# Kernel optimization log

Measured on AMD Instinct MI355X. Metric: run time of the kernel, lower is better.

Reference implementation:

```python
import jax, jax.numpy as jnp
import numpy as np


def setup_inputs() -> dict:
    key = jax.random.key(0)
    k1, k2, k3 = jax.random.split(key, 3)
    x = jax.random.normal(k1, (128, 3, 16, 64, 64), dtype=jnp.float32)
    conv_weight = jax.random.normal(k2, (24, 3, 3, 3, 3), dtype=jnp.float32) * 0.1
    conv_bias = jax.random.normal(k3, (24,), dtype=jnp.float32) * 0.1
    return {"x": x, "conv_weight": conv_weight, "conv_bias": conv_bias}


def reference(x, conv_weight, conv_bias):
    # Conv3d, stride=1, padding=0 (VALID), dilation=1, groups=1, NCDHW layout
    y = jax.lax.conv_general_dilated(
        x, conv_weight,
        window_strides=(1, 1, 1),
        padding='VALID',
        dimension_numbers=('NCDHW', 'OIDHW', 'NCDHW'),
    )
    y = y + conv_bias[None, :, None, None, None]  # [B, 24, 14, 62, 62]
    y = jnp.min(y, axis=2)                        # min over depth -> [B, 24, 62, 62]
    return jax.nn.softmax(y, axis=1)              # softmax over channels
```

## Files before the change

kernel.cpp:

```cpp
#include <hip/hip_runtime.h>
#include <math.h>

#define BATCH 128
#define CIN   3
#define DIN   16
#define HWIN  64
#define COUT  24
#define DOUT  14
#define HOUT  62
#define WOUT  62


__global__ __launch_bounds__(192, 3) void conv_min_softmax_v2(
    const float* __restrict__ x,
    const float* __restrict__ w,
    const float* __restrict__ bias,
    float* __restrict__ out)
{
    __shared__ __align__(16) float sx[3][9][68];
    __shared__ float sm[COUT][64];

    const int tid = threadIdx.x;
    const int bid = blockIdx.x;
    const int ho  = bid % HOUT;
    const int b   = bid / HOUT;

    const int co = tid >> 3;
    const int wg = tid & 7;

    const float* xb = x + (size_t)b * (CIN * DIN * HWIN * HWIN);

    float wreg[81];
    #pragma unroll
    for (int q = 0; q < 81; ++q) wreg[q] = w[co * 81 + q];
    const float bco = bias[co];

    const int r  = tid >> 6;
    const int wc = tid & 63;

    #pragma unroll
    for (int d = 0; d < 2; ++d) {
        #pragma unroll
        for (int cin = 0; cin < CIN; ++cin) {
            sx[d][cin * 3 + r][wc] =
                xb[(cin * DIN + d) * (HWIN * HWIN) + (ho + r) * HWIN + wc];
        }
    }

    float m[8];
    #pragma unroll
    for (int i = 0; i < 8; ++i) m[i] = 1e30f;

    #pragma unroll 1
    for (int dz = 0; dz < DOUT; ++dz) {
        const int s2 = (dz + 2) % 3;
        #pragma unroll
        for (int cin = 0; cin < CIN; ++cin) {
            sx[s2][cin * 3 + r][wc] =
                xb[(cin * DIN + dz + 2) * (HWIN * HWIN) + (ho + r) * HWIN + wc];
        }
        __syncthreads();

        const int p0 = dz % 3;
        const int p1 = (dz + 1) % 3;
        const float* planes[3] = { &sx[p0][0][0], &sx[p1][0][0], &sx[s2][0][0] };

        float acc[8];
        #pragma unroll
        for (int i = 0; i < 8; ++i) acc[i] = 0.f;

        #pragma unroll
        for (int kd = 0; kd < 3; ++kd) {
            const float* plane = planes[kd];
            #pragma unroll
            for (int cin = 0; cin < CIN; ++cin) {
                #pragma unroll
                for (int kh = 0; kh < 3; ++kh) {
                    const float* rp = plane + (cin * 3 + kh) * 68 + wg * 8;
                    float xr[10];
                    const float4 q0 = *(const float4*)(rp);
                    const float4 q1 = *(const float4*)(rp + 4);
                    const float2 q2 = *(const float2*)(rp + 8);
                    xr[0] = q0.x; xr[1] = q0.y; xr[2] = q0.z; xr[3] = q0.w;
                    xr[4] = q1.x; xr[5] = q1.y; xr[6] = q1.z; xr[7] = q1.w;
                    xr[8] = q2.x; xr[9] = q2.y;
                    #pragma unroll
                    for (int kw = 0; kw < 3; ++kw) {
                        const float wv = wreg[cin * 27 + kd * 9 + kh * 3 + kw];
                        #pragma unroll
                        for (int i = 0; i < 8; ++i)
                            acc[i] = fmaf(wv, xr[i + kw], acc[i]);
                    }
                }
            }
        }
        #pragma unroll
        for (int i = 0; i < 8; ++i) m[i] = fminf(m[i], acc[i]);
        __syncthreads();
    }

    #pragma unroll
    for (int i = 0; i < 8; ++i) sm[co][wg * 8 + i] = m[i] + bco;
    __syncthreads();

    if (tid < WOUT) {
        const int p = tid;
        float mx = -1e30f;
        #pragma unroll
        for (int c = 0; c < COUT; ++c) mx = fmaxf(mx, sm[c][p]);
        float e[COUT];
        float ssum = 0.f;
        #pragma unroll
        for (int c = 0; c < COUT; ++c) { e[c] = __expf(sm[c][p] - mx); ssum += e[c]; }
        const float inv = 1.f / ssum;
        float* ob = out + (size_t)b * COUT * (HOUT * WOUT) + ho * WOUT + p;
        #pragma unroll
        for (int c = 0; c < COUT; ++c) ob[(size_t)c * (HOUT * WOUT)] = e[c] * inv;
    }
}

extern "C" void kernel_launch(void* const* d_in, const int* in_sizes, int n_in,
                              void* d_out, int out_size, void* d_ws, size_t ws_size,
                              hipStream_t stream) {
    const float* x    = (const float*)d_in[0];
    const float* w    = (const float*)d_in[1];
    const float* bias = (const float*)d_in[2];
    float* out = (float*)d_out;

    const int blocks = BATCH * HOUT;
    conv_min_softmax_v2<<<blocks, 192, 0, stream>>>(x, w, bias, out);
}
```

Measured before the change: 457.0 us.

## Stream input depth planes once with rolling accumulators and register prefetch

The kernel now loads each input depth plane into shared memory once and applies all three depth taps of the weights to it. Three rolling accumulator sets (A0/A1/A2) are shifted after each plane instead of re-reading three planes per output depth. Global loads for the next plane are prefetched into registers while the current plane is computed, which overlaps load latency with math. Shared-memory reads drop by about 3x, but live registers grow (three 8-wide accumulators plus 81 weights) and the volatile weight loads may hurt occupancy or scheduling.

```diff
diff --git a/kernel.cpp b/kernel.cpp
--- a/kernel.cpp
+++ b/kernel.cpp
@@ -9,16 +9,56 @@
 #define DOUT  14
 #define HOUT  62
 #define WOUT  62
+#define HW2   (HWIN * HWIN)
 
 
-__global__ __launch_bounds__(192, 3) void conv_min_softmax_v2(
+template<bool KD0, bool KD1, bool KD2>
+__device__ __forceinline__ void conv_step(const float* sxp, int wg,
+                                          const float wreg[81],
+                                          float A0[8], float A1[8], float A2[8])
+{
+    #pragma unroll
+    for (int cin = 0; cin < 3; ++cin) {
+        #pragma unroll
+        for (int kh = 0; kh < 3; ++kh) {
+            const float* rp = sxp + (cin * 3 + kh) * 68 + wg * 8;
+            float xr[10];
+            const float4 q0 = *(const float4*)(rp);
+            const float4 q1 = *(const float4*)(rp + 4);
+            const float2 q2 = *(const float2*)(rp + 8);
+            xr[0] = q0.x; xr[1] = q0.y; xr[2] = q0.z; xr[3] = q0.w;
+            xr[4] = q1.x; xr[5] = q1.y; xr[6] = q1.z; xr[7] = q1.w;
+            xr[8] = q2.x; xr[9] = q2.y;
+            #pragma unroll
+            for (int kw = 0; kw < 3; ++kw) {
+                if (KD2) {
+                    const float wv = wreg[cin * 27 + 2 * 9 + kh * 3 + kw];
+                    #pragma unroll
+                    for (int i = 0; i < 8; ++i) A0[i] = fmaf(wv, xr[i + kw], A0[i]);
+                }
+                if (KD1) {
+                    const float wv = wreg[cin * 27 + 1 * 9 + kh * 3 + kw];
+                    #pragma unroll
+                    for (int i = 0; i < 8; ++i) A1[i] = fmaf(wv, xr[i + kw], A1[i]);
+                }
+                if (KD0) {
+                    const float wv = wreg[cin * 27 + 0 * 9 + kh * 3 + kw];
+                    #pragma unroll
+                    for (int i = 0; i < 8; ++i) A2[i] = fmaf(wv, xr[i + kw], A2[i]);
+                }
+            }
+        }
+    }
+}
+
+__global__ __launch_bounds__(192, 3) void conv_min_softmax_v3(
     const float* __restrict__ x,
     const float* __restrict__ w,
     const float* __restrict__ bias,
     float* __restrict__ out)
 {
-    __shared__ __align__(16) float sx[3][9][68];
-    __shared__ float sm[COUT][64];
+    __shared__ __align__(16) float sx[9 * 68];
+    __shared__ __align__(16) float sm[COUT][68];
 
     const int tid = threadIdx.x;
     const int bid = blockIdx.x;
@@ -28,76 +68,78 @@
     const int co = tid >> 3;
     const int wg = tid & 7;
 
-    const float* xb = x + (size_t)b * (CIN * DIN * HWIN * HWIN);
+    const float* xb = x + (size_t)b * (CIN * DIN * HW2);
 
     float wreg[81];
-    #pragma unroll
-    for (int q = 0; q < 81; ++q) wreg[q] = w[co * 81 + q];
+    {
+        volatile const float* wv = w + co * 81;
+        #pragma unroll
+        for (int q = 0; q < 81; ++q) wreg[q] = wv[q];
+    }
     const float bco = bias[co];
 
     const int r  = tid >> 6;
     const int wc = tid & 63;
 
+    float A0[8], A1[8], A2[8], m[8];
     #pragma unroll
-    for (int d = 0; d < 2; ++d) {
+    for (int i = 0; i < 8; ++i) { A0[i] = 0.f; A1[i] = 0.f; A2[i] = 0.f; m[i] = 1e30f; }
+
+    float g0, g1, g2, n0, n1, n2;
+    g0 = xb[(0 * DIN + 0) * HW2 + (ho + r) * HWIN + wc];
+    g1 = xb[(1 * DIN + 0) * HW2 + (ho + r) * HWIN + wc];
+    g2 = xb[(2 * DIN + 0) * HW2 + (ho + r) * HWIN + wc];
+
+#define STAGE_AND_PREFETCH(D)                                              \
+    sx[(0 * 3 + r) * 68 + wc] = g0;                                        \
+    sx[(1 * 3 + r) * 68 + wc] = g1;                                        \
+    sx[(2 * 3 + r) * 68 + wc] = g2;                                        \
+    if ((D) < DIN - 1) {                                                   \
+        n0 = xb[(0 * DIN + (D) + 1) * HW2 + (ho + r) * HWIN + wc];         \
+        n1 = xb[(1 * DIN + (D) + 1) * HW2 + (ho + r) * HWIN + wc];         \
+        n2 = xb[(2 * DIN + (D) + 1) * HW2 + (ho + r) * HWIN + wc];         \
+    }                                                                      \
+    __syncthreads();
+
+#define SHIFT()                                                            \
+    _Pragma("unroll")                                                      \
+    for (int i = 0; i < 8; ++i) { A0[i] = A1[i]; A1[i] = A2[i]; A2[i] = 0.f; } \
+    g0 = n0; g1 = n1; g2 = n2;
+
+    STAGE_AND_PREFETCH(0)
+    conv_step<true, false, false>(sx, wg, wreg, A0, A1, A2);
+    SHIFT()
+    __syncthreads();
+
+    STAGE_AND_PREFETCH(1)
+    conv_step<true, true, false>(sx, wg, wreg, A0, A1, A2);
+    SHIFT()
+    __syncthreads();
+
+    #pragma unroll 1
+    for (int d = 2; d <= 13; ++d) {
+        STAGE_AND_PREFETCH(d)
+        conv_step<true, true, true>(sx, wg, wreg, A0, A1, A2);
         #pragma unroll
-        for (int cin = 0; cin < CIN; ++cin) {
-            sx[d][cin * 3 + r][wc] =
-                xb[(cin * DIN + d) * (HWIN * HWIN) + (ho + r) * HWIN + wc];
-        }
+        for (int i = 0; i < 8; ++i) m[i] = fminf(m[i], A0[i]);
+        SHIFT()
+        __syncthreads();
     }
 
-    float m[8];
+    STAGE_AND_PREFETCH(14)
+    conv_step<false, true, true>(sx, wg, wreg, A0, A1, A2);
     #pragma unroll
-    for (int i = 0; i < 8; ++i) m[i] = 1e30f;
+    for (int i = 0; i < 8; ++i) m[i] = fminf(m[i], A0[i]);
+    SHIFT()
+    __syncthreads();
 
-    #pragma unroll 1
-    for (int dz = 0; dz < DOUT; ++dz) {
-        const int s2 = (dz + 2) % 3;
-        #pragma unroll
-        for (int cin = 0; cin < CIN; ++cin) {
-            sx[s2][cin * 3 + r][wc] =
-                xb[(cin * DIN + dz + 2) * (HWIN * HWIN) + (ho + r) * HWIN + wc];
-        }
-        __syncthreads();
+    STAGE_AND_PREFETCH(15)
+    conv_step<false, false, true>(sx, wg, wreg, A0, A1, A2);
+    #pragma unroll
+    for (int i = 0; i < 8; ++i) m[i] = fminf(m[i], A0[i]);
 
-        const int p0 = dz % 3;
-        const int p1 = (dz + 1) % 3;
-        const float* planes[3] = { &sx[p0][0][0], &sx[p1][0][0], &sx[s2][0][0] };
-
-        float acc[8];
-        #pragma unroll
-        for (int i = 0; i < 8; ++i) acc[i] = 0.f;
-
-        #pragma unroll
-        for (int kd = 0; kd < 3; ++kd) {
-            const float* plane = planes[kd];
-            #pragma unroll
-            for (int cin = 0; cin < CIN; ++cin) {
-                #pragma unroll
-                for (int kh = 0; kh < 3; ++kh) {
-                    const float* rp = plane + (cin * 3 + kh) * 68 + wg * 8;
-                    float xr[10];
-                    const float4 q0 = *(const float4*)(rp);
-                    const float4 q1 = *(const float4*)(rp + 4);
-                    const float2 q2 = *(const float2*)(rp + 8);
-                    xr[0] = q0.x; xr[1] = q0.y; xr[2] = q0.z; xr[3] = q0.w;
-                    xr[4] = q1.x; xr[5] = q1.y; xr[6] = q1.z; xr[7] = q1.w;
-                    xr[8] = q2.x; xr[9] = q2.y;
-                    #pragma unroll
-                    for (int kw = 0; kw < 3; ++kw) {
-                        const float wv = wreg[cin * 27 + kd * 9 + kh * 3 + kw];
-                        #pragma unroll
-                        for (int i = 0; i < 8; ++i)
-                            acc[i] = fmaf(wv, xr[i + kw], acc[i]);
-                    }
-                }
-            }
-        }
-        #pragma unroll
-        for (int i = 0; i < 8; ++i) m[i] = fminf(m[i], acc[i]);
-        __syncthreads();
-    }
+#undef STAGE_AND_PREFETCH
+#undef SHIFT
 
     #pragma unroll
     for (int i = 0; i < 8; ++i) sm[co][wg * 8 + i] = m[i] + bco;
@@ -128,5 +170,5 @@
     float* out = (float*)d_out;
 
     const int blocks = BATCH * HOUT;
-    conv_min_softmax_v2<<<blocks, 192, 0, stream>>>(x, w, bias, out);
+    conv_min_softmax_v3<<<blocks, 192, 0, stream>>>(x, w, bias, out);
 }
```

Result: slower. 666.0 us (+45.7%).

## Stream input depth planes once with rotating output accumulators and register prefetch

Applied to the files above, without the earlier changes.

Each input depth plane is staged into shared memory once and scattered into the three output-depth accumulators it feeds, replacing the three-plane ring buffer that re-read every plane three times. The next plane's global loads are prefetched into registers while the current one is computed. Weights are now read from global or constant-cached memory inside the loop instead of being held in 81 registers, which frees registers but adds scalar or cached loads per FMA group. The shared softmax buffer is padded to 65 columns to avoid bank conflicts.

```diff
diff --git a/kernel.cpp b/kernel.cpp
--- a/kernel.cpp
+++ b/kernel.cpp
@@ -9,16 +9,18 @@
 #define DOUT  14
 #define HOUT  62
 #define WOUT  62
+#define HW2   (HWIN * HWIN)
+#define RS    68
 
 
-__global__ __launch_bounds__(192, 3) void conv_min_softmax_v2(
+__global__ __launch_bounds__(192, 3) void conv_min_softmax_v7(
     const float* __restrict__ x,
     const float* __restrict__ w,
     const float* __restrict__ bias,
     float* __restrict__ out)
 {
-    __shared__ __align__(16) float sx[3][9][68];
-    __shared__ float sm[COUT][64];
+    __shared__ __align__(16) float sx[9 * RS];
+    __shared__ float sm[COUT][65];
 
     const int tid = threadIdx.x;
     const int bid = blockIdx.x;
@@ -28,77 +30,119 @@
     const int co = tid >> 3;
     const int wg = tid & 7;
 
-    const float* xb = x + (size_t)b * (CIN * DIN * HWIN * HWIN);
-
-    float wreg[81];
-    #pragma unroll
-    for (int q = 0; q < 81; ++q) wreg[q] = w[co * 81 + q];
-    const float bco = bias[co];
+    const float* xb  = x + (size_t)b * (CIN * DIN * HW2);
+    const float* wco = w + co * 81;
 
     const int r  = tid >> 6;
     const int wc = tid & 63;
 
+    const int gb0 = (0 * DIN) * HW2 + (ho + r) * HWIN + wc;
+    const int gb1 = (1 * DIN) * HW2 + (ho + r) * HWIN + wc;
+    const int gb2 = (2 * DIN) * HW2 + (ho + r) * HWIN + wc;
+
+    float X0[8], X1[8], X2[8], m[8];
     #pragma unroll
-    for (int d = 0; d < 2; ++d) {
-        #pragma unroll
-        for (int cin = 0; cin < CIN; ++cin) {
-            sx[d][cin * 3 + r][wc] =
-                xb[(cin * DIN + d) * (HWIN * HWIN) + (ho + r) * HWIN + wc];
-        }
+    for (int i = 0; i < 8; ++i) { X0[i] = 0.f; X1[i] = 0.f; X2[i] = 0.f; m[i] = 1e30f; }
+
+    float g0 = xb[gb0], g1 = xb[gb1], g2 = xb[gb2];
+    float n0, n1, n2;
+    int doff = HW2;
+
+#define STAGE(LAST)                                                        \
+    sx[(0 * 3 + r) * RS + wc] = g0;                                        \
+    sx[(1 * 3 + r) * RS + wc] = g1;                                        \
+    sx[(2 * 3 + r) * RS + wc] = g2;                                        \
+    if (!(LAST)) { n0 = xb[gb0 + doff]; n1 = xb[gb1 + doff]; n2 = xb[gb2 + doff]; } \
+    __syncthreads();
+
+#define ENDP()                                                             \
+    __syncthreads();                                                       \
+    g0 = n0; g1 = n1; g2 = n2; doff += HW2;
+
+#define PLANE(SB, S1, S2, DB, D1, D2)                                      \
+    {                                                                      \
+        _Pragma("unroll")                                                  \
+        for (int cin = 0; cin < 3; ++cin) {                                \
+            _Pragma("unroll")                                              \
+            for (int kh = 0; kh < 3; ++kh) {                               \
+                const float* rp = sx + (cin * 3 + kh) * RS + wg * 8;       \
+                float xr[10];                                              \
+                {                                                          \
+                    const float4 q0 = *(const float4*)(rp);                \
+                    const float4 q1 = *(const float4*)(rp + 4);            \
+                    const float2 q2 = *(const float2*)(rp + 8);            \
+                    xr[0] = q0.x; xr[1] = q0.y; xr[2] = q0.z; xr[3] = q0.w;\
+                    xr[4] = q1.x; xr[5] = q1.y; xr[6] = q1.z; xr[7] = q1.w;\
+                    xr[8] = q2.x; xr[9] = q2.y;                            \
+                }                                                          \
+                _Pragma("unroll")                                          \
+                for (int kw = 0; kw < 3; ++kw) {                           \
+                    if (DB) {                                              \
+                        const float wv = wco[cin * 27 + 0 * 9 + kh * 3 + kw]; \
+                        _Pragma("unroll")                                  \
+                        for (int i = 0; i < 8; ++i)                        \
+                            SB[i] = fmaf(wv, xr[i + kw], SB[i]);           \
+                    }                                                      \
+                    if (D1) {                                              \
+                        const float wv = wco[cin * 27 + 1 * 9 + kh * 3 + kw]; \
+                        _Pragma("unroll")                                  \
+                        for (int i = 0; i < 8; ++i)                        \
+                            S1[i] = fmaf(wv, xr[i + kw], S1[i]);           \
+                    }                                                      \
+                    if (D2) {                                              \
+                        const float wv = wco[cin * 27 + 2 * 9 + kh * 3 + kw]; \
+                        _Pragma("unroll")                                  \
+                        for (int i = 0; i < 8; ++i)                        \
+                            S2[i] = fmaf(wv, xr[i + kw], S2[i]);           \
+                    }                                                      \
+                }                                                          \
+            }                                                              \
+        }                                                                  \
     }
 
-    float m[8];
-    #pragma unroll
-    for (int i = 0; i < 8; ++i) m[i] = 1e30f;
+#define MINRESET(S)                                                        \
+    _Pragma("unroll")                                                      \
+    for (int i = 0; i < 8; ++i) { m[i] = fminf(m[i], S[i]); S[i] = 0.f; }
+
+    STAGE(0)
+    PLANE(X0, X1, X2, 1, 0, 0)
+    ENDP()
+
+    STAGE(0)
+    PLANE(X1, X0, X2, 1, 1, 0)
+    ENDP()
 
     #pragma unroll 1
-    for (int dz = 0; dz < DOUT; ++dz) {
-        const int s2 = (dz + 2) % 3;
-        #pragma unroll
-        for (int cin = 0; cin < CIN; ++cin) {
-            sx[s2][cin * 3 + r][wc] =
-                xb[(cin * DIN + dz + 2) * (HWIN * HWIN) + (ho + r) * HWIN + wc];
-        }
-        __syncthreads();
-
-        const int p0 = dz % 3;
-        const int p1 = (dz + 1) % 3;
-        const float* planes[3] = { &sx[p0][0][0], &sx[p1][0][0], &sx[s2][0][0] };
-
-        float acc[8];
-        #pragma unroll
-        for (int i = 0; i < 8; ++i) acc[i] = 0.f;
-
-        #pragma unroll
-        for (int kd = 0; kd < 3; ++kd) {
-            const float* plane = planes[kd];
-            #pragma unroll
-            for (int cin = 0; cin < CIN; ++cin) {
-                #pragma unroll
-                for (int kh = 0; kh < 3; ++kh) {
-                    const float* rp = plane + (cin * 3 + kh) * 68 + wg * 8;
-                    float xr[10];
-                    const float4 q0 = *(const float4*)(rp);
-                    const float4 q1 = *(const float4*)(rp + 4);
-                    const float2 q2 = *(const float2*)(rp + 8);
-                    xr[0] = q0.x; xr[1] = q0.y; xr[2] = q0.z; xr[3] = q0.w;
-                    xr[4] = q1.x; xr[5] = q1.y; xr[6] = q1.z; xr[7] = q1.w;
-                    xr[8] = q2.x; xr[9] = q2.y;
-                    #pragma unroll
-                    for (int kw = 0; kw < 3; ++kw) {
-                        const float wv = wreg[cin * 27 + kd * 9 + kh * 3 + kw];
-                        #pragma unroll
-                        for (int i = 0; i < 8; ++i)
-                            acc[i] = fmaf(wv, xr[i + kw], acc[i]);
-                    }
-                }
-            }
-        }
-        #pragma unroll
-        for (int i = 0; i < 8; ++i) m[i] = fminf(m[i], acc[i]);
-        __syncthreads();
+    for (int d3 = 0; d3 < 4; ++d3) {
+        STAGE(0)
+        PLANE(X2, X1, X0, 1, 1, 1)
+        MINRESET(X0)
+        ENDP()
+        STAGE(0)
+        PLANE(X0, X2, X1, 1, 1, 1)
+        MINRESET(X1)
+        ENDP()
+        STAGE(0)
+        PLANE(X1, X0, X2, 1, 1, 1)
+        MINRESET(X2)
+        ENDP()
     }
 
+    STAGE(0)
+    PLANE(X2, X1, X0, 0, 1, 1)
+    MINRESET(X0)
+    ENDP()
+
+    STAGE(1)
+    PLANE(X2, X0, X1, 0, 0, 1)
+    MINRESET(X1)
+
+#undef STAGE
+#undef ENDP
+#undef PLANE
+#undef MINRESET
+
+    const float bco = bias[co];
     #pragma unroll
     for (int i = 0; i < 8; ++i) sm[co][wg * 8 + i] = m[i] + bco;
     __syncthreads();
@@ -128,5 +172,5 @@
     float* out = (float*)d_out;
 
     const int blocks = BATCH * HOUT;
-    conv_min_softmax_v2<<<blocks, 192, 0, stream>>>(x, w, bias, out);
+    conv_min_softmax_v7<<<blocks, 192, 0, stream>>>(x, w, bias, out);
 }
```

After: 1.042 ms. 2.28x slower.
